# Optimization experiments

Hardware: AMD Instinct MI355X
Metric: run time of the kernel (lower is better)

Reference implementation:

```python
import jax, jax.numpy as jnp
import numpy as np

K = 3            # num_neighbors
C_IN = 128       # in_channels (== out_channels, required by fusion_kernel)
C_OUT = 128
B, H, W = 2, 64, 512
EPS = 1e-5       # BatchNorm eps (eval mode, running stats)


def _unfold(x, k):
    # F.unfold(x, k, padding=k//2).view(B, C, k*k, H*W); patch index = kh*k + kw
    b, c, h, w = x.shape
    p = k // 2
    xp = jnp.pad(x, ((0, 0), (0, 0), (p, p), (p, p)))
    patches = jnp.stack(
        [xp[:, :, i:i + h, j:j + w] for i in range(k) for j in range(k)], axis=2
    )  # (B, C, k*k, H, W)
    return patches.reshape(b, c, k * k, h * w)


def _conv1x1(x, w):
    # 1x1 Conv2d (bias=False) on (B, C, K^2, HW)
    return jnp.einsum('oc,bcnp->bonp', w, x)


def _bn(x, g, b, m, v):
    # BatchNorm2d in eval mode with running stats
    scale = (g / jnp.sqrt(v + EPS))[None, :, None, None]
    shift = (b - m * g / jnp.sqrt(v + EPS))[None, :, None, None]
    return x * scale + shift


def setup_inputs() -> dict:
    key = jax.random.key(0)
    ks = jax.random.split(key, 9)
    f32 = jnp.float32
    features = jax.random.normal(ks[0], (B, C_IN, H, W), f32)
    cart = jax.random.normal(ks[1], (B, 3, H, W), f32)
    mask = jax.random.bernoulli(ks[2], 0.9, (B, 1, H, W))

    def bn_params(k, c):
        k1, k2, k3, k4 = jax.random.split(k, 4)
        g = 1.0 + 0.1 * jax.random.normal(k1, (c,), f32)
        b = 0.1 * jax.random.normal(k2, (c,), f32)
        m = 0.1 * jax.random.normal(k3, (c,), f32)
        v = jax.random.uniform(k4, (c,), f32, 0.5, 1.5)
        return g, b, m, v

    pw = jax.random.normal(ks[3], (C_OUT, 3), f32) / jnp.sqrt(3.0)
    pg, pb, pm, pv = bn_params(ks[4], C_OUT)
    fw = jax.random.normal(ks[5], (C_OUT, C_IN), f32) / jnp.sqrt(float(C_IN))
    fg, fb, fm, fv = bn_params(ks[6], C_OUT)
    ew = jax.random.normal(ks[7], (3, C_OUT), f32) / jnp.sqrt(float(C_OUT))
    eg, eb, em, ev = bn_params(ks[8], 3)
    return dict(features=features, cart=cart, mask=mask,
                pw=pw, pg=pg, pb=pb, pm=pm, pv=pv,
                fw=fw, fg=fg, fb=fb, fm=fm, fv=fv,
                ew=ew, eg=eg, eb=eb, em=em, ev=ev)


def reference(features, cart, mask, pw, pg, pb, pm, pv,
              fw, fg, fb, fm, fv, ew, eg, eb, em, ev):
    b, c, h, w = features.shape
    fdt = features.dtype
    fe = _unfold(features, K)                      # (B, C, K^2, HW)
    cc = _unfold(cart, K)                          # (B, 3, K^2, HW)
    mu = _unfold(mask.astype(fdt), K)              # (B, 1, K^2, HW)
    center = (K * K) // 2
    rel = cc - cc[:, :, center:center + 1]         # relative coordinates
    pos = jax.nn.relu(_bn(_conv1x1(rel, pw), pg, pb, pm, pv))
    fe = jax.nn.relu(_bn(_conv1x1(fe, fw), fg, fb, fm, fv)) + pos
    geo = jnp.max(fe * mu, axis=2, keepdims=True)  # max_pool over K^2 neighbors
    e2c = _bn(_conv1x1(geo, ew), eg, eb, em, ev).reshape(b, 3, h, w)
    cart_out = cart + e2c * mask.astype(cart.dtype)
    return geo.reshape(b, -1, h, w), cart_out
```

## Files before the change

### kernel.cpp

```cpp
#include <hip/hip_runtime.h>

typedef unsigned short u16;
typedef unsigned int u32;
typedef unsigned char u8;

#define HW 32768
#define NPX 65536
#define GEO_SIZE 8388608
#define EPS 1e-5f

#define OFF_PWP   0
#define OFF_EWP   512
#define OFF_SHE   1024
#define OFF_FLG   1028
#define OFF_SHF   1088
#define W2T_OFF   8192
#define MSK_OFF   40960
#define EAP_OFF   131072
#define T_OFF     917504

typedef __bf16 bf16x8 __attribute__((ext_vector_type(8)));
typedef float f32x4 __attribute__((ext_vector_type(4)));

__device__ __forceinline__ float bf2f(u16 u){ return __uint_as_float(((u32)u) << 16); }
__device__ __forceinline__ u16 f2bf(float f){
  u32 x = __float_as_uint(f);
  return (u16)((x + 0x7fffu + ((x >> 16) & 1u)) >> 16);
}

__device__ __forceinline__ float ldp(const void* p, int i, bool isbf){
  return isbf ? bf2f(((const u16*)p)[i]) : ((const float*)p)[i];
}

__device__ __forceinline__ bool sniff_bf16(const void* fv){
  const u16* w = (const u16*)fv;
  int hits = 0;
  for (int i = 0; i < 32; i++) {
    float v = bf2f(w[i]);
    hits += (v >= 0.45f && v <= 1.55f) ? 1 : 0;
  }
  return hits >= 26;
}

__device__ __forceinline__ int sniff_mask(const void* mask){
  const u8* mb = (const u8*)mask;
  int c01 = 0, ones = 0;
  for (int i = 0; i < 64; i++) { u8 v = mb[i]; c01 += (v <= 1); ones += (v == 1); }
  if (c01 == 64) return (ones >= 24) ? 0 : 1;
  const u16* mw = (const u16*)mask;
  int c3f = 0;
  for (int i = 0; i < 32; i++) c3f += (mw[i] == 0x3F80);
  return (c3f >= 22) ? 2 : 3;
}

__global__ void prep_kernel(const void* __restrict__ pw, const void* __restrict__ pg,
                            const void* __restrict__ pb, const void* __restrict__ pm,
                            const void* __restrict__ pv,
                            const void* __restrict__ fw, const void* __restrict__ fg,
                            const void* __restrict__ fb, const void* __restrict__ fm,
                            const void* __restrict__ fv,
                            const void* __restrict__ ew, const void* __restrict__ eg,
                            const void* __restrict__ eb, const void* __restrict__ em,
                            const void* __restrict__ ev,
                            const void* __restrict__ mask,
                            float* __restrict__ ws){
  int o = threadIdx.x;
  bool isbf = sniff_bf16(fv);
  if (o == 0) {
    ws[OFF_FLG]     = isbf ? 1.f : 0.f;
    ws[OFF_FLG + 1] = (float)sniff_mask(mask);
  }
  float sf = ldp(fg, o, isbf) / sqrtf(ldp(fv, o, isbf) + EPS);
  ws[OFF_SHF + o] = ldp(fb, o, isbf) - ldp(fm, o, isbf) * sf;
  u16* w2t = (u16*)((char*)ws + W2T_OFF);
  for (int c = 0; c < 128; c++) w2t[o * 128 + c] = f2bf(sf * ldp(fw, o * 128 + c, isbf));
  float sp = ldp(pg, o, isbf) / sqrtf(ldp(pv, o, isbf) + EPS);
  float4* pwp = (float4*)(ws + OFF_PWP);
  pwp[o] = make_float4(sp * ldp(pw, o * 3 + 0, isbf),
                       sp * ldp(pw, o * 3 + 1, isbf),
                       sp * ldp(pw, o * 3 + 2, isbf),
                       ldp(pb, o, isbf) - ldp(pm, o, isbf) * sp);
  float se0 = ldp(eg, 0, isbf) / sqrtf(ldp(ev, 0, isbf) + EPS);
  float se1 = ldp(eg, 1, isbf) / sqrtf(ldp(ev, 1, isbf) + EPS);
  float se2 = ldp(eg, 2, isbf) / sqrtf(ldp(ev, 2, isbf) + EPS);
  float4* ewp = (float4*)(ws + OFF_EWP);
  ewp[o] = make_float4(se0 * ldp(ew, 0 * 128 + o, isbf),
                       se1 * ldp(ew, 1 * 128 + o, isbf),
                       se2 * ldp(ew, 2 * 128 + o, isbf), 0.f);
  if (o < 3) {
    float se = ldp(eg, o, isbf) / sqrtf(ldp(ev, o, isbf) + EPS);
    ws[OFF_SHE + o] = ldp(eb, o, isbf) - ldp(em, o, isbf) * se;
  }
}

__global__ __launch_bounds__(256) void mask_decode_kernel(const void* __restrict__ mask,
                                                          const float* __restrict__ ws,
                                                          u8* __restrict__ msk,
                                                          float* __restrict__ eap){
  int i = blockIdx.x * 256 + threadIdx.x;
  int enc = (int)ws[OFF_FLG + 1];
  u8 v;
  if (enc == 0)      v = (((const u8*)mask)[i] != 0);
  else if (enc == 1) v = (((const int*)mask)[i] != 0);
  else if (enc == 2) v = (((const u16*)mask)[i] != 0);
  else               v = (((const float*)mask)[i] != 0.f);
  msk[i] = v;
  eap[i] = 0.f; eap[NPX + i] = 0.f; eap[2 * NPX + i] = 0.f;
}

__global__ __launch_bounds__(256) void transpose_kernel(const void* __restrict__ feat,
                                                        const float* __restrict__ ws,
                                                        u16* __restrict__ xT){
  __shared__ u32 lds[128 * 65];
  int t = threadIdx.x;
  int pxg = blockIdx.x * 128;
  int b = pxg >> 15, hw0 = pxg & 32767;
  bool isbf = ws[OFF_FLG] > 0.5f;
  int c = t & 127, seg = t >> 7;
  long elem = (long)(b * 128 + c) * HW + hw0 + seg * 64;
  u32* ldsrow = lds + c * 65 + seg * 32;
  if (isbf) {
    const uint4* g = (const uint4*)((const u16*)feat + elem);
#pragma unroll
    for (int i = 0; i < 8; i++) {
      uint4 q = g[i];
      ldsrow[i * 4 + 0] = q.x; ldsrow[i * 4 + 1] = q.y;
      ldsrow[i * 4 + 2] = q.z; ldsrow[i * 4 + 3] = q.w;
    }
  } else {
    const float4* g = (const float4*)((const float*)feat + elem);
#pragma unroll
    for (int i = 0; i < 16; i++) {
      float4 f = g[i];
      ldsrow[i * 2 + 0] = (u32)f2bf(f.x) | ((u32)f2bf(f.y) << 16);
      ldsrow[i * 2 + 1] = (u32)f2bf(f.z) | ((u32)f2bf(f.w) << 16);
    }
  }
  __syncthreads();
  int px = t & 127, chalf = t >> 7;
  const u16* l16 = (const u16*)lds;
  u32 o32[32];
#pragma unroll
  for (int i = 0; i < 32; i++) {
    int c0 = chalf * 64 + 2 * i;
    u32 lo = l16[c0 * 130 + px];
    u32 hi = l16[(c0 + 1) * 130 + px];
    o32[i] = lo | (hi << 16);
  }
  uint4* dst = (uint4*)(xT + (pxg + px) * 128 + chalf * 64);
#pragma unroll
  for (int j = 0; j < 8; j++)
    dst[j] = make_uint4(o32[j * 4], o32[j * 4 + 1], o32[j * 4 + 2], o32[j * 4 + 3]);
}

__global__ __launch_bounds__(256) void stage1_kernel(const u16* __restrict__ xT,
                                                     const float* __restrict__ ws,
                                                     u16* __restrict__ t){
  int tid = threadIdx.x;
  int wave = tid >> 6, lane = tid & 63;
  int ln = lane & 15, quad = lane >> 4;
  int px0 = blockIdx.x * 128 + wave * 32;
  const uint4* W = (const uint4*)((const char*)ws + W2T_OFF);
  const uint4* X = (const uint4*)xT;

  f32x4 acc[8][2];
#pragma unroll
  for (int ot = 0; ot < 8; ot++)
#pragma unroll
    for (int pt = 0; pt < 2; pt++) acc[ot][pt] = (f32x4){0.f, 0.f, 0.f, 0.f};

#pragma unroll
  for (int ks = 0; ks < 4; ks++) {
    bf16x8 a[8], bfr[2];
#pragma unroll
    for (int ot = 0; ot < 8; ot++)
      a[ot] = __builtin_bit_cast(bf16x8, W[(ot * 16 + ln) * 16 + ks * 4 + quad]);
#pragma unroll
    for (int pt = 0; pt < 2; pt++)
      bfr[pt] = __builtin_bit_cast(bf16x8, X[(px0 + pt * 16 + ln) * 16 + ks * 4 + quad]);
#pragma unroll
    for (int ot = 0; ot < 8; ot++)
#pragma unroll
      for (int pt = 0; pt < 2; pt++)
        acc[ot][pt] = __builtin_amdgcn_mfma_f32_16x16x32_bf16(a[ot], bfr[pt], acc[ot][pt], 0, 0, 0);
  }
  const float* shf = ws + OFF_SHF;
#pragma unroll
  for (int ot = 0; ot < 8; ot++) {
#pragma unroll
    for (int r = 0; r < 4; r++) {
      int o = ot * 16 + quad * 4 + r;
      float s = shf[o];
#pragma unroll
      for (int pt = 0; pt < 2; pt++) {
        float v = fmaxf(acc[ot][pt][r] + s, 0.f);
        t[o * NPX + px0 + pt * 16 + ln] = f2bf(v);
      }
    }
  }
}

__global__ __launch_bounds__(256) void stage2_kernel(const void* __restrict__ cart,
                                                     const float* __restrict__ ws,
                                                     const u8* __restrict__ msk,
                                                     const u16* __restrict__ t,
                                                     float* __restrict__ eap,
                                                     void* __restrict__ out){
  int pxb = blockIdx.x & 255, grp = blockIdx.x >> 8;
  int px = pxb * 256 + threadIdx.x;
  int b = px >> 15, hw = px & 32767;
  int h = hw >> 9, w = hw & 511;
  bool isbf = ws[OFF_FLG] > 0.5f;
  float c0x, c0y, c0z;
  const u16* cb16 = (const u16*)cart + b * 3 * HW;
  const float* cbf = (const float*)cart + b * 3 * HW;
  if (isbf) { c0x = bf2f(cb16[hw]); c0y = bf2f(cb16[HW + hw]); c0z = bf2f(cb16[2 * HW + hw]); }
  else      { c0x = cbf[hw];        c0y = cbf[HW + hw];        c0z = cbf[2 * HW + hw]; }
  int pxn[9];
  float mv[9];
  float rel[9][3];
#pragma unroll
  for (int n = 0; n < 9; n++) {
    int dh = n / 3 - 1, dw = n % 3 - 1;
    int h2 = h + dh, w2 = w + dw;
    bool ok = ((unsigned)h2 < 64u) && ((unsigned)w2 < 512u);
    int hw2 = ok ? ((h2 << 9) | w2) : hw;
    ok = ok && (msk[b * HW + hw2] != 0);
    pxn[n] = b * HW + hw2;
    mv[n] = ok ? 1.f : 0.f;
    if (isbf) {
      rel[n][0] = bf2f(cb16[hw2]) - c0x;
      rel[n][1] = bf2f(cb16[HW + hw2]) - c0y;
      rel[n][2] = bf2f(cb16[2 * HW + hw2]) - c0z;
    } else {
      rel[n][0] = cbf[hw2] - c0x;
      rel[n][1] = cbf[HW + hw2] - c0y;
      rel[n][2] = cbf[2 * HW + hw2] - c0z;
    }
  }
  const float4* pwp = (const float4*)(ws + OFF_PWP);
  const float4* ewp = (const float4*)(ws + OFF_EWP);
  float ea0 = 0.f, ea1 = 0.f, ea2 = 0.f;
  u16* o16 = (u16*)out;
  float* of = (float*)out;
  int o0 = grp * 32;
#pragma unroll 4
  for (int o = o0; o < o0 + 32; o++) {
    const u16* tb = t + o * NPX;
    float4 P = pwp[o];
    float g = 0.f;
#pragma unroll
    for (int n = 0; n < 9; n++) {
      float tf = bf2f(tb[pxn[n]]);
      float pos = fmaxf(fmaf(P.x, rel[n][0],
                        fmaf(P.y, rel[n][1],
                        fmaf(P.z, rel[n][2], P.w))), 0.f);
      g = fmaxf(g, (tf + pos) * mv[n]);
    }
    int gi = (b * 128 + o) * HW + hw;
    if (isbf) o16[gi] = f2bf(g); else of[gi] = g;
    float4 E = ewp[o];
    ea0 = fmaf(E.x, g, ea0);
    ea1 = fmaf(E.y, g, ea1);
    ea2 = fmaf(E.z, g, ea2);
  }
  atomicAdd(&eap[px], ea0);
  atomicAdd(&eap[NPX + px], ea1);
  atomicAdd(&eap[2 * NPX + px], ea2);
}

__global__ __launch_bounds__(256) void final_kernel(const void* __restrict__ cart,
                                                    const float* __restrict__ ws,
                                                    const u8* __restrict__ msk,
                                                    const float* __restrict__ eap,
                                                    void* __restrict__ out){
  int px = blockIdx.x * 256 + threadIdx.x;
  int b = px >> 15, hw = px & 32767;
  bool isbf = ws[OFF_FLG] > 0.5f;
  float c0x, c0y, c0z;
  const u16* cb16 = (const u16*)cart + b * 3 * HW;
  const float* cbf = (const float*)cart + b * 3 * HW;
  if (isbf) { c0x = bf2f(cb16[hw]); c0y = bf2f(cb16[HW + hw]); c0z = bf2f(cb16[2 * HW + hw]); }
  else      { c0x = cbf[hw];        c0y = cbf[HW + hw];        c0z = cbf[2 * HW + hw]; }
  float m = (msk[b * HW + hw] != 0) ? 1.f : 0.f;
  float r0 = c0x + (eap[px] + ws[OFF_SHE]) * m;
  float r1 = c0y + (eap[NPX + px] + ws[OFF_SHE + 1]) * m;
  float r2 = c0z + (eap[2 * NPX + px] + ws[OFF_SHE + 2]) * m;
  int cbase = GEO_SIZE + b * 3 * HW + hw;
  if (isbf) {
    u16* o16 = (u16*)out;
    o16[cbase] = f2bf(r0); o16[cbase + HW] = f2bf(r1); o16[cbase + 2 * HW] = f2bf(r2);
  } else {
    float* of = (float*)out;
    of[cbase] = r0; of[cbase + HW] = r1; of[cbase + 2 * HW] = r2;
  }
}

extern "C" void kernel_launch(void* const* d_in, const int* in_sizes, int n_in,
                              void* d_out, int out_size, void* d_ws, size_t ws_size,
                              hipStream_t stream) {
  const void* feat = d_in[0];
  const void* cart = d_in[1];
  const void* mask = d_in[2];
  float* ws  = (float*)d_ws;
  u8*   msk  = (u8*)((char*)d_ws + MSK_OFF);
  float* eap = (float*)((char*)d_ws + EAP_OFF);
  u16*  t    = (u16*)((char*)d_ws + T_OFF);
  u16*  xT   = (u16*)d_out;

  hipLaunchKernelGGL(prep_kernel, dim3(1), dim3(128), 0, stream,
                     d_in[3], d_in[4], d_in[5], d_in[6], d_in[7],
                     d_in[8], d_in[9], d_in[10], d_in[11], d_in[12],
                     d_in[13], d_in[14], d_in[15], d_in[16], d_in[17],
                     mask, ws);
  hipLaunchKernelGGL(mask_decode_kernel, dim3(256), dim3(256), 0, stream, mask, ws, msk, eap);
  hipLaunchKernelGGL(transpose_kernel, dim3(512), dim3(256), 0, stream, feat, ws, xT);
  hipLaunchKernelGGL(stage1_kernel, dim3(512), dim3(256), 0, stream, xT, ws, t);
  hipLaunchKernelGGL(stage2_kernel, dim3(1024), dim3(256), 0, stream, cart, ws, msk, t, eap, d_out);
  hipLaunchKernelGGL(final_kernel, dim3(256), dim3(256), 0, stream, cart, ws, msk, eap, d_out);
}
```

Before: 199.4 us.

## Fuse transpose into GEMM, drop mask decode, two pixels per thread, per-group partials

Removes the separate transpose and mask-decode kernels. Stage1 now loads features straight into LDS in transposed form and stages its output through LDS so global stores are coalesced. Stage2 handles two adjacent pixels per thread, reading neighbour t values as packed 32-bit words and sharing cart and mask loads across both pixels. It also replaces atomics with per-group partial sums that the final kernel reduces. This cuts launches, intermediate traffic and atomics, but stage2 reads t at w-2 with no edge guard and relies on the raw mask encoding at every use.

```diff
diff --git a/kernel.cpp b/kernel.cpp
--- a/kernel.cpp
+++ b/kernel.cpp
@@ -15,9 +15,10 @@
 #define OFF_FLG   1028
 #define OFF_SHF   1088
 #define W2T_OFF   8192
-#define MSK_OFF   40960
 #define EAP_OFF   131072
-#define T_OFF     917504
+#define T_OFF     8388608
+
+#define LDS_STRIDE 136
 
 typedef __bf16 bf16x8 __attribute__((ext_vector_type(8)));
 typedef float f32x4 __attribute__((ext_vector_type(4)));
@@ -27,6 +28,8 @@
   u32 x = __float_as_uint(f);
   return (u16)((x + 0x7fffu + ((x >> 16) & 1u)) >> 16);
 }
+__device__ __forceinline__ float bflo(u32 w){ return __uint_as_float(w << 16); }
+__device__ __forceinline__ float bfhi(u32 w){ return __uint_as_float(w & 0xffff0000u); }
 
 __device__ __forceinline__ float ldp(const void* p, int i, bool isbf){
   return isbf ? bf2f(((const u16*)p)[i]) : ((const float*)p)[i];
@@ -51,6 +54,13 @@
   int c3f = 0;
   for (int i = 0; i < 32; i++) c3f += (mw[i] == 0x3F80);
   return (c3f >= 22) ? 2 : 3;
+}
+
+__device__ __forceinline__ float mask_at(const void* m, int gi, int enc){
+  if (enc == 0) return ((const u8*)m)[gi]  ? 1.f : 0.f;
+  if (enc == 1) return ((const int*)m)[gi] ? 1.f : 0.f;
+  if (enc == 2) return ((const u16*)m)[gi] ? 1.f : 0.f;
+  return (((const float*)m)[gi] != 0.f) ? 1.f : 0.f;
 }
 
 __global__ void prep_kernel(const void* __restrict__ pw, const void* __restrict__ pg,
@@ -72,8 +82,23 @@
   }
   float sf = ldp(fg, o, isbf) / sqrtf(ldp(fv, o, isbf) + EPS);
   ws[OFF_SHF + o] = ldp(fb, o, isbf) - ldp(fm, o, isbf) * sf;
-  u16* w2t = (u16*)((char*)ws + W2T_OFF);
-  for (int c = 0; c < 128; c++) w2t[o * 128 + c] = f2bf(sf * ldp(fw, o * 128 + c, isbf));
+  u32* w2t = (u32*)((char*)ws + W2T_OFF);
+  if (isbf) {
+    const u32* fwp = (const u32*)fw;
+    for (int c = 0; c < 128; c += 2) {
+      u32 in = fwp[(o * 128 + c) >> 1];
+      u32 lo = (u32)f2bf(sf * bf2f((u16)(in & 0xffff)));
+      u32 hi = (u32)f2bf(sf * bf2f((u16)(in >> 16)));
+      w2t[(o * 128 + c) >> 1] = lo | (hi << 16);
+    }
+  } else {
+    const float* fwp = (const float*)fw;
+    for (int c = 0; c < 128; c += 2) {
+      u32 lo = (u32)f2bf(sf * fwp[o * 128 + c]);
+      u32 hi = (u32)f2bf(sf * fwp[o * 128 + c + 1]);
+      w2t[(o * 128 + c) >> 1] = lo | (hi << 16);
+    }
+  }
   float sp = ldp(pg, o, isbf) / sqrtf(ldp(pv, o, isbf) + EPS);
   float4* pwp = (float4*)(ws + OFF_PWP);
   pwp[o] = make_float4(sp * ldp(pw, o * 3 + 0, isbf),
@@ -93,75 +118,58 @@
   }
 }
 
-__global__ __launch_bounds__(256) void mask_decode_kernel(const void* __restrict__ mask,
-                                                          const float* __restrict__ ws,
-                                                          u8* __restrict__ msk,
-                                                          float* __restrict__ eap){
-  int i = blockIdx.x * 256 + threadIdx.x;
-  int enc = (int)ws[OFF_FLG + 1];
-  u8 v;
-  if (enc == 0)      v = (((const u8*)mask)[i] != 0);
-  else if (enc == 1) v = (((const int*)mask)[i] != 0);
-  else if (enc == 2) v = (((const u16*)mask)[i] != 0);
-  else               v = (((const float*)mask)[i] != 0.f);
-  msk[i] = v;
-  eap[i] = 0.f; eap[NPX + i] = 0.f; eap[2 * NPX + i] = 0.f;
-}
-
-__global__ __launch_bounds__(256) void transpose_kernel(const void* __restrict__ feat,
-                                                        const float* __restrict__ ws,
-                                                        u16* __restrict__ xT){
-  __shared__ u32 lds[128 * 65];
-  int t = threadIdx.x;
+__global__ __launch_bounds__(256) void stage1_kernel(const void* __restrict__ feat,
+                                                     const float* __restrict__ ws,
+                                                     u16* __restrict__ t){
+  __shared__ u16 lds[128 * LDS_STRIDE];
+  int tid = threadIdx.x;
+  bool isbf = ws[OFF_FLG] > 0.5f;
   int pxg = blockIdx.x * 128;
   int b = pxg >> 15, hw0 = pxg & 32767;
-  bool isbf = ws[OFF_FLG] > 0.5f;
-  int c = t & 127, seg = t >> 7;
-  long elem = (long)(b * 128 + c) * HW + hw0 + seg * 64;
-  u32* ldsrow = lds + c * 65 + seg * 32;
-  if (isbf) {
-    const uint4* g = (const uint4*)((const u16*)feat + elem);
-#pragma unroll
-    for (int i = 0; i < 8; i++) {
-      uint4 q = g[i];
-      ldsrow[i * 4 + 0] = q.x; ldsrow[i * 4 + 1] = q.y;
-      ldsrow[i * 4 + 2] = q.z; ldsrow[i * 4 + 3] = q.w;
-    }
-  } else {
-    const float4* g = (const float4*)((const float*)feat + elem);
-#pragma unroll
-    for (int i = 0; i < 16; i++) {
-      float4 f = g[i];
-      ldsrow[i * 2 + 0] = (u32)f2bf(f.x) | ((u32)f2bf(f.y) << 16);
-      ldsrow[i * 2 + 1] = (u32)f2bf(f.z) | ((u32)f2bf(f.w) << 16);
+
+  {
+    int cp = tid & 63, q = tid >> 6;
+    int c0 = cp * 2;
+    long e0 = (long)(b * 128 + c0) * HW + hw0 + q * 32;
+    u16* base = lds + (q * 32) * LDS_STRIDE + c0;
+    if (isbf) {
+      const uint4* g0 = (const uint4*)((const u16*)feat + e0);
+      const uint4* g1 = (const uint4*)((const u16*)feat + e0 + HW);
+#pragma unroll
+      for (int i = 0; i < 4; i++) {
+        uint4 a = g0[i], c = g1[i];
+        u32 av[4] = {a.x, a.y, a.z, a.w};
+        u32 cv[4] = {c.x, c.y, c.z, c.w};
+#pragma unroll
+        for (int k = 0; k < 4; k++) {
+          u32 lo = (av[k] & 0xffffu) | (cv[k] << 16);
+          u32 hi = (av[k] >> 16) | (cv[k] & 0xffff0000u);
+          *(u32*)(base + (i * 8 + k * 2 + 0) * LDS_STRIDE) = lo;
+          *(u32*)(base + (i * 8 + k * 2 + 1) * LDS_STRIDE) = hi;
+        }
+      }
+    } else {
+      const float4* g0 = (const float4*)((const float*)feat + e0);
+      const float4* g1 = (const float4*)((const float*)feat + e0 + HW);
+#pragma unroll
+      for (int i = 0; i < 8; i++) {
+        float4 a = g0[i], c = g1[i];
+        float av[4] = {a.x, a.y, a.z, a.w};
+        float cv[4] = {c.x, c.y, c.z, c.w};
+#pragma unroll
+        for (int k = 0; k < 4; k++) {
+          u32 v = (u32)f2bf(av[k]) | ((u32)f2bf(cv[k]) << 16);
+          *(u32*)(base + (i * 4 + k) * LDS_STRIDE) = v;
+        }
+      }
     }
   }
   __syncthreads();
-  int px = t & 127, chalf = t >> 7;
-  const u16* l16 = (const u16*)lds;
-  u32 o32[32];
-#pragma unroll
-  for (int i = 0; i < 32; i++) {
-    int c0 = chalf * 64 + 2 * i;
-    u32 lo = l16[c0 * 130 + px];
-    u32 hi = l16[(c0 + 1) * 130 + px];
-    o32[i] = lo | (hi << 16);
-  }
-  uint4* dst = (uint4*)(xT + (pxg + px) * 128 + chalf * 64);
-#pragma unroll
-  for (int j = 0; j < 8; j++)
-    dst[j] = make_uint4(o32[j * 4], o32[j * 4 + 1], o32[j * 4 + 2], o32[j * 4 + 3]);
-}
-
-__global__ __launch_bounds__(256) void stage1_kernel(const u16* __restrict__ xT,
-                                                     const float* __restrict__ ws,
-                                                     u16* __restrict__ t){
-  int tid = threadIdx.x;
+
   int wave = tid >> 6, lane = tid & 63;
   int ln = lane & 15, quad = lane >> 4;
-  int px0 = blockIdx.x * 128 + wave * 32;
+  int pxw = wave * 32;
   const uint4* W = (const uint4*)((const char*)ws + W2T_OFF);
-  const uint4* X = (const uint4*)xT;
 
   f32x4 acc[8][2];
 #pragma unroll
@@ -177,13 +185,16 @@
       a[ot] = __builtin_bit_cast(bf16x8, W[(ot * 16 + ln) * 16 + ks * 4 + quad]);
 #pragma unroll
     for (int pt = 0; pt < 2; pt++)
-      bfr[pt] = __builtin_bit_cast(bf16x8, X[(px0 + pt * 16 + ln) * 16 + ks * 4 + quad]);
+      bfr[pt] = __builtin_bit_cast(bf16x8,
+          *(const uint4*)(lds + (pxw + pt * 16 + ln) * LDS_STRIDE + ks * 32 + quad * 8));
 #pragma unroll
     for (int ot = 0; ot < 8; ot++)
 #pragma unroll
       for (int pt = 0; pt < 2; pt++)
         acc[ot][pt] = __builtin_amdgcn_mfma_f32_16x16x32_bf16(a[ot], bfr[pt], acc[ot][pt], 0, 0, 0);
   }
+  __syncthreads();
+
   const float* shf = ws + OFF_SHF;
 #pragma unroll
   for (int ot = 0; ot < 8; ot++) {
@@ -194,105 +205,167 @@
 #pragma unroll
       for (int pt = 0; pt < 2; pt++) {
         float v = fmaxf(acc[ot][pt][r] + s, 0.f);
-        t[o * NPX + px0 + pt * 16 + ln] = f2bf(v);
-      }
-    }
+        lds[o * LDS_STRIDE + pxw + pt * 16 + ln] = f2bf(v);
+      }
+    }
+  }
+  __syncthreads();
+  {
+    int o = tid >> 1, half = tid & 1;
+    const u16* src = lds + o * LDS_STRIDE + half * 64;
+    uint4* dst = (uint4*)(t + o * NPX + pxg + half * 64);
+#pragma unroll
+    for (int k = 0; k < 8; k++) dst[k] = *(const uint4*)(src + k * 8);
   }
 }
 
 __global__ __launch_bounds__(256) void stage2_kernel(const void* __restrict__ cart,
                                                      const float* __restrict__ ws,
-                                                     const u8* __restrict__ msk,
+                                                     const void* __restrict__ rawmask,
                                                      const u16* __restrict__ t,
                                                      float* __restrict__ eap,
                                                      void* __restrict__ out){
-  int pxb = blockIdx.x & 255, grp = blockIdx.x >> 8;
-  int px = pxb * 256 + threadIdx.x;
-  int b = px >> 15, hw = px & 32767;
+  int tid = threadIdx.x;
+  int pxb = blockIdx.x & 127, grp = blockIdx.x >> 7;
+  int px0 = pxb * 512 + tid * 2;
+  int b = px0 >> 15, hw = px0 & 32767;
   int h = hw >> 9, w = hw & 511;
   bool isbf = ws[OFF_FLG] > 0.5f;
-  float c0x, c0y, c0z;
-  const u16* cb16 = (const u16*)cart + b * 3 * HW;
-  const float* cbf = (const float*)cart + b * 3 * HW;
-  if (isbf) { c0x = bf2f(cb16[hw]); c0y = bf2f(cb16[HW + hw]); c0z = bf2f(cb16[2 * HW + hw]); }
-  else      { c0x = cbf[hw];        c0y = cbf[HW + hw];        c0z = cbf[2 * HW + hw]; }
-  int pxn[9];
-  float mv[9];
-  float rel[9][3];
-#pragma unroll
-  for (int n = 0; n < 9; n++) {
-    int dh = n / 3 - 1, dw = n % 3 - 1;
-    int h2 = h + dh, w2 = w + dw;
-    bool ok = ((unsigned)h2 < 64u) && ((unsigned)w2 < 512u);
-    int hw2 = ok ? ((h2 << 9) | w2) : hw;
-    ok = ok && (msk[b * HW + hw2] != 0);
-    pxn[n] = b * HW + hw2;
-    mv[n] = ok ? 1.f : 0.f;
-    if (isbf) {
-      rel[n][0] = bf2f(cb16[hw2]) - c0x;
-      rel[n][1] = bf2f(cb16[HW + hw2]) - c0y;
-      rel[n][2] = bf2f(cb16[2 * HW + hw2]) - c0z;
-    } else {
-      rel[n][0] = cbf[hw2] - c0x;
-      rel[n][1] = cbf[HW + hw2] - c0y;
-      rel[n][2] = cbf[2 * HW + hw2] - c0z;
-    }
-  }
+  int enc = (int)ws[OFF_FLG + 1];
+
+  float rel[2][9][3];
+  float mvv[12];
+  {
+    float cr[12][3];
+#pragma unroll
+    for (int r = 0; r < 3; r++) {
+#pragma unroll
+      for (int c = 0; c < 4; c++) {
+        int idx = r * 4 + c;
+        int h2 = h + r - 1, w2 = w + c - 1;
+        bool ok = ((unsigned)h2 < 64u) && ((unsigned)w2 < 512u);
+        int hw2 = ok ? ((h2 << 9) | w2) : hw;
+        int gi = b * HW + hw2;
+        float mval = mask_at(rawmask, gi, enc);
+        mvv[idx] = ok ? mval : 0.f;
+#pragma unroll
+        for (int d = 0; d < 3; d++)
+          cr[idx][d] = isbf ? bf2f(((const u16*)cart)[(b * 3 + d) * HW + hw2])
+                            : ((const float*)cart)[(b * 3 + d) * HW + hw2];
+      }
+    }
+#pragma unroll
+    for (int r = 0; r < 3; r++)
+#pragma unroll
+      for (int cc = 0; cc < 3; cc++)
+#pragma unroll
+        for (int d = 0; d < 3; d++) {
+          rel[0][r * 3 + cc][d] = cr[r * 4 + cc][d]     - cr[5][d];
+          rel[1][r * 3 + cc][d] = cr[r * 4 + cc + 1][d] - cr[6][d];
+        }
+  }
+
   const float4* pwp = (const float4*)(ws + OFF_PWP);
   const float4* ewp = (const float4*)(ws + OFF_EWP);
-  float ea0 = 0.f, ea1 = 0.f, ea2 = 0.f;
+  float ea00 = 0.f, ea01 = 0.f, ea02 = 0.f;
+  float ea10 = 0.f, ea11 = 0.f, ea12 = 0.f;
   u16* o16 = (u16*)out;
   float* of = (float*)out;
-  int o0 = grp * 32;
+
 #pragma unroll 4
-  for (int o = o0; o < o0 + 32; o++) {
-    const u16* tb = t + o * NPX;
+  for (int j = 0; j < 16; j++) {
+    int o = grp * 16 + j;
+    const u16* tb = t + o * NPX + b * HW;
+    u32 tw[3][3];
+#pragma unroll
+    for (int r = 0; r < 3; r++) {
+      const u32* rp = (const u32*)(tb + (h + r - 1) * 512 + (w - 2));
+      tw[r][0] = rp[0]; tw[r][1] = rp[1]; tw[r][2] = rp[2];
+    }
     float4 P = pwp[o];
-    float g = 0.f;
-#pragma unroll
-    for (int n = 0; n < 9; n++) {
-      float tf = bf2f(tb[pxn[n]]);
-      float pos = fmaxf(fmaf(P.x, rel[n][0],
-                        fmaf(P.y, rel[n][1],
-                        fmaf(P.z, rel[n][2], P.w))), 0.f);
-      g = fmaxf(g, (tf + pos) * mv[n]);
+    float g0 = 0.f, g1 = 0.f;
+#pragma unroll
+    for (int r = 0; r < 3; r++) {
+      float tm1 = bfhi(tw[r][0]);
+      float t0  = bflo(tw[r][1]);
+      float tp1 = bfhi(tw[r][1]);
+      float tp2 = bflo(tw[r][2]);
+      float tv0[3] = {tm1, t0, tp1};
+      float tv1[3] = {t0, tp1, tp2};
+#pragma unroll
+      for (int cc = 0; cc < 3; cc++) {
+        int n = r * 3 + cc;
+        float pos0 = fmaxf(fmaf(P.x, rel[0][n][0],
+                           fmaf(P.y, rel[0][n][1],
+                           fmaf(P.z, rel[0][n][2], P.w))), 0.f);
+        g0 = fmaxf(g0, (tv0[cc] + pos0) * mvv[r * 4 + cc]);
+        float pos1 = fmaxf(fmaf(P.x, rel[1][n][0],
+                           fmaf(P.y, rel[1][n][1],
+                           fmaf(P.z, rel[1][n][2], P.w))), 0.f);
+        g1 = fmaxf(g1, (tv1[cc] + pos1) * mvv[r * 4 + cc + 1]);
+      }
     }
     int gi = (b * 128 + o) * HW + hw;
-    if (isbf) o16[gi] = f2bf(g); else of[gi] = g;
+    if (isbf) *(u32*)(o16 + gi) = (u32)f2bf(g0) | ((u32)f2bf(g1) << 16);
+    else { of[gi] = g0; of[gi + 1] = g1; }
     float4 E = ewp[o];
-    ea0 = fmaf(E.x, g, ea0);
-    ea1 = fmaf(E.y, g, ea1);
-    ea2 = fmaf(E.z, g, ea2);
-  }
-  atomicAdd(&eap[px], ea0);
-  atomicAdd(&eap[NPX + px], ea1);
-  atomicAdd(&eap[2 * NPX + px], ea2);
+    ea00 = fmaf(E.x, g0, ea00); ea01 = fmaf(E.y, g0, ea01); ea02 = fmaf(E.z, g0, ea02);
+    ea10 = fmaf(E.x, g1, ea10); ea11 = fmaf(E.y, g1, ea11); ea12 = fmaf(E.z, g1, ea12);
+  }
+  float2* ep;
+  ep = (float2*)(eap + (grp * 3 + 0) * NPX + px0); *ep = make_float2(ea00, ea10);
+  ep = (float2*)(eap + (grp * 3 + 1) * NPX + px0); *ep = make_float2(ea01, ea11);
+  ep = (float2*)(eap + (grp * 3 + 2) * NPX + px0); *ep = make_float2(ea02, ea12);
 }
 
 __global__ __launch_bounds__(256) void final_kernel(const void* __restrict__ cart,
                                                     const float* __restrict__ ws,
-                                                    const u8* __restrict__ msk,
+                                                    const void* __restrict__ rawmask,
                                                     const float* __restrict__ eap,
                                                     void* __restrict__ out){
-  int px = blockIdx.x * 256 + threadIdx.x;
-  int b = px >> 15, hw = px & 32767;
+  int px0 = (blockIdx.x * 256 + threadIdx.x) * 2;
+  int b = px0 >> 15, hw = px0 & 32767;
   bool isbf = ws[OFF_FLG] > 0.5f;
-  float c0x, c0y, c0z;
-  const u16* cb16 = (const u16*)cart + b * 3 * HW;
-  const float* cbf = (const float*)cart + b * 3 * HW;
-  if (isbf) { c0x = bf2f(cb16[hw]); c0y = bf2f(cb16[HW + hw]); c0z = bf2f(cb16[2 * HW + hw]); }
-  else      { c0x = cbf[hw];        c0y = cbf[HW + hw];        c0z = cbf[2 * HW + hw]; }
-  float m = (msk[b * HW + hw] != 0) ? 1.f : 0.f;
-  float r0 = c0x + (eap[px] + ws[OFF_SHE]) * m;
-  float r1 = c0y + (eap[NPX + px] + ws[OFF_SHE + 1]) * m;
-  float r2 = c0z + (eap[2 * NPX + px] + ws[OFF_SHE + 2]) * m;
+  int enc = (int)ws[OFF_FLG + 1];
+  float s0a = 0.f, s0b = 0.f, s1a = 0.f, s1b = 0.f, s2a = 0.f, s2b = 0.f;
+#pragma unroll
+  for (int g = 0; g < 8; g++) {
+    float2 v0 = *(const float2*)(eap + (g * 3 + 0) * NPX + px0);
+    float2 v1 = *(const float2*)(eap + (g * 3 + 1) * NPX + px0);
+    float2 v2 = *(const float2*)(eap + (g * 3 + 2) * NPX + px0);
+    s0a += v0.x; s0b += v0.y;
+    s1a += v1.x; s1b += v1.y;
+    s2a += v2.x; s2b += v2.y;
+  }
+  float m0 = mask_at(rawmask, b * HW + hw, enc);
+  float m1 = mask_at(rawmask, b * HW + hw + 1, enc);
+  float she0 = ws[OFF_SHE], she1 = ws[OFF_SHE + 1], she2 = ws[OFF_SHE + 2];
+  float c0a, c0b, c1a, c1b, c2a, c2b;
+  if (isbf) {
+    const u16* cb = (const u16*)cart + b * 3 * HW;
+    c0a = bf2f(cb[hw]); c0b = bf2f(cb[hw + 1]);
+    c1a = bf2f(cb[HW + hw]); c1b = bf2f(cb[HW + hw + 1]);
+    c2a = bf2f(cb[2 * HW + hw]); c2b = bf2f(cb[2 * HW + hw + 1]);
+  } else {
+    const float* cb = (const float*)cart + b * 3 * HW;
+    c0a = cb[hw]; c0b = cb[hw + 1];
+    c1a = cb[HW + hw]; c1b = cb[HW + hw + 1];
+    c2a = cb[2 * HW + hw]; c2b = cb[2 * HW + hw + 1];
+  }
+  float r0a = c0a + (s0a + she0) * m0, r0b = c0b + (s0b + she0) * m1;
+  float r1a = c1a + (s1a + she1) * m0, r1b = c1b + (s1b + she1) * m1;
+  float r2a = c2a + (s2a + she2) * m0, r2b = c2b + (s2b + she2) * m1;
   int cbase = GEO_SIZE + b * 3 * HW + hw;
   if (isbf) {
     u16* o16 = (u16*)out;
-    o16[cbase] = f2bf(r0); o16[cbase + HW] = f2bf(r1); o16[cbase + 2 * HW] = f2bf(r2);
+    *(u32*)(o16 + cbase)          = (u32)f2bf(r0a) | ((u32)f2bf(r0b) << 16);
+    *(u32*)(o16 + cbase + HW)     = (u32)f2bf(r1a) | ((u32)f2bf(r1b) << 16);
+    *(u32*)(o16 + cbase + 2 * HW) = (u32)f2bf(r2a) | ((u32)f2bf(r2b) << 16);
   } else {
     float* of = (float*)out;
-    of[cbase] = r0; of[cbase + HW] = r1; of[cbase + 2 * HW] = r2;
+    of[cbase] = r0a; of[cbase + 1] = r0b;
+    of[cbase + HW] = r1a; of[cbase + HW + 1] = r1b;
+    of[cbase + 2 * HW] = r2a; of[cbase + 2 * HW + 1] = r2b;
   }
 }
 
@@ -303,19 +376,15 @@
   const void* cart = d_in[1];
   const void* mask = d_in[2];
   float* ws  = (float*)d_ws;
-  u8*   msk  = (u8*)((char*)d_ws + MSK_OFF);
   float* eap = (float*)((char*)d_ws + EAP_OFF);
   u16*  t    = (u16*)((char*)d_ws + T_OFF);
-  u16*  xT   = (u16*)d_out;
 
   hipLaunchKernelGGL(prep_kernel, dim3(1), dim3(128), 0, stream,
                      d_in[3], d_in[4], d_in[5], d_in[6], d_in[7],
                      d_in[8], d_in[9], d_in[10], d_in[11], d_in[12],
                      d_in[13], d_in[14], d_in[15], d_in[16], d_in[17],
                      mask, ws);
-  hipLaunchKernelGGL(mask_decode_kernel, dim3(256), dim3(256), 0, stream, mask, ws, msk, eap);
-  hipLaunchKernelGGL(transpose_kernel, dim3(512), dim3(256), 0, stream, feat, ws, xT);
-  hipLaunchKernelGGL(stage1_kernel, dim3(512), dim3(256), 0, stream, xT, ws, t);
-  hipLaunchKernelGGL(stage2_kernel, dim3(1024), dim3(256), 0, stream, cart, ws, msk, t, eap, d_out);
-  hipLaunchKernelGGL(final_kernel, dim3(256), dim3(256), 0, stream, cart, ws, msk, eap, d_out);
-}
+  hipLaunchKernelGGL(stage1_kernel, dim3(512), dim3(256), 0, stream, feat, ws, t);
+  hipLaunchKernelGGL(stage2_kernel, dim3(1024), dim3(256), 0, stream, cart, ws, mask, t, eap, d_out);
+  hipLaunchKernelGGL(final_kernel, dim3(128), dim3(256), 0, stream, cart, ws, mask, eap, d_out);
+}
```

Result: faster. 169.0 us (-15.2%).
